# Kernel optimization log

Hardware: AMD Instinct MI355X
Metric: run time of the kernel (lower is better)

The kernel has to match this reference:

```python
import jax, jax.numpy as jnp
import numpy as np

K_HEADS, D_HEAD = 8, 8
D = K_HEADS * D_HEAD  # 64


def _fc(x, W, b=None, relu=False):
    # 1x1 Conv2D over (B,T,N,C) == per-position dense
    y = x @ W
    if b is not None:
        y = y + b
    return jax.nn.relu(y) if relu else y


def _split_heads(x):
    # (B,T,N,K*d) -> (K,B,T,N,d); matches torch.cat(torch.split(x, d, -1), 0)
    B, T, N, _ = x.shape
    return x.reshape(B, T, N, K_HEADS, D_HEAD).transpose(3, 0, 1, 2, 4)


def _merge_heads(x):
    # (K,B,T,N,d) -> (B,T,N,K*d); matches torch.cat(torch.split(x, B, 0), -1)
    K, B, T, N, d = x.shape
    return x.transpose(1, 2, 3, 0, 4).reshape(B, T, N, K * d)


def _forward(X, TLE, key_padding_mask, *P):
    (sa_Wq, sa_bq, sa_Wk, sa_bk, sa_Wv, sa_bv, sa_Wo1, sa_bo1, sa_Wo2, sa_bo2,
     ta_Wq, ta_bq, ta_Wk, ta_bk, ta_Wv, ta_bv, ta_Wo1, ta_bo1, ta_Wo2, ta_bo2,
     g_Wxs, g_Wxt, g_bxt, g_Wh1, g_bh1, g_Wh2, g_bh2) = P
    B, T, N, _ = X.shape
    scale = 1.0 / (D_HEAD ** 0.5)
    XE = jnp.concatenate([X, TLE], axis=-1)  # (B,T,N,3D)

    # ---- Spatial attention (over nodes) ----
    q = _split_heads(_fc(XE, sa_Wq, sa_bq, True))
    k = _split_heads(_fc(XE, sa_Wk, sa_bk, True))
    v = _split_heads(_fc(XE, sa_Wv, sa_bv, True))
    s = jnp.einsum('kbtnd,kbtmd->kbtnm', q, k) * scale  # (K,B,T,N,N)
    p = jax.nn.softmax(s, axis=-1)
    HS = _merge_heads(jnp.einsum('kbtnm,kbtmd->kbtnd', p, v))
    HS = _fc(_fc(HS, sa_Wo1, sa_bo1, True), sa_Wo2, sa_bo2)

    # ---- Temporal attention (over time, causal + key padding) ----
    q = _split_heads(_fc(XE, ta_Wq, ta_bq, True))
    k = _split_heads(_fc(XE, ta_Wk, ta_bk, True))
    v = _split_heads(_fc(XE, ta_Wv, ta_bv, True))
    s = jnp.einsum('kbind,kbjnd->kbnij', q, k) * scale  # (K,B,N,T,T)
    causal = jnp.tril(jnp.ones((T, T), dtype=bool))  # (T,T)
    valid_key = jnp.arange(T)[None, :] < key_padding_mask  # (B,T)
    m = causal[None, None, None] & valid_key[None, :, None, None, :]
    s = jnp.where(m, s, -jnp.inf)
    p = jax.nn.softmax(s, axis=-1)
    HT = _merge_heads(jnp.einsum('kbnij,kbjnd->kbind', p, v))
    HT = _fc(_fc(HT, ta_Wo1, ta_bo1, True), ta_Wo2, ta_bo2)

    # ---- Gated fusion + residual ----
    z = jax.nn.sigmoid(HS @ g_Wxs + HT @ g_Wxt + g_bxt)
    H = z * HS + (1.0 - z) * HT
    H = _fc(_fc(H, g_Wh1, g_bh1, True), g_Wh2, g_bh2)
    return X + H


_PARAM_SHAPES = []
for _pre in ('sa', 'ta'):
    _PARAM_SHAPES += [(_pre + '_Wq', (3 * D, D)), (_pre + '_bq', (D,)),
                      (_pre + '_Wk', (3 * D, D)), (_pre + '_bk', (D,)),
                      (_pre + '_Wv', (3 * D, D)), (_pre + '_bv', (D,)),
                      (_pre + '_Wo1', (D, D)), (_pre + '_bo1', (D,)),
                      (_pre + '_Wo2', (D, D)), (_pre + '_bo2', (D,))]
_PARAM_SHAPES += [('g_Wxs', (D, D)), ('g_Wxt', (D, D)), ('g_bxt', (D,)),
                  ('g_Wh1', (D, D)), ('g_bh1', (D,)),
                  ('g_Wh2', (D, D)), ('g_bh2', (D,))]


def setup_inputs() -> dict:
    key = jax.random.key(0)
    ks = jax.random.split(key, 3 + len(_PARAM_SHAPES))
    B, T, N = 16, 24, 128
    inp = {
        'X': jax.random.normal(ks[0], (B, T, N, D), dtype=jnp.float32),
        'TLE': jax.random.normal(ks[1], (B, T, N, 2 * D), dtype=jnp.float32),
        'key_padding_mask': jax.random.randint(ks[2], (B, 1), 1, T + 1),
    }
    for i, (nm, shp) in enumerate(_PARAM_SHAPES):
        inp[nm] = jax.random.normal(ks[3 + i], shp, dtype=jnp.float32) * 0.05
    return inp


def reference(X, TLE, key_padding_mask,
              sa_Wq, sa_bq, sa_Wk, sa_bk, sa_Wv, sa_bv, sa_Wo1, sa_bo1, sa_Wo2, sa_bo2,
              ta_Wq, ta_bq, ta_Wk, ta_bk, ta_Wv, ta_bv, ta_Wo1, ta_bo1, ta_Wo2, ta_bo2,
              g_Wxs, g_Wxt, g_bxt, g_Wh1, g_bh1, g_Wh2, g_bh2):
    return _forward(X, TLE, key_padding_mask,
                    sa_Wq, sa_bq, sa_Wk, sa_bk, sa_Wv, sa_bv, sa_Wo1, sa_bo1, sa_Wo2, sa_bo2,
                    ta_Wq, ta_bq, ta_Wk, ta_bk, ta_Wv, ta_bv, ta_Wo1, ta_bo1, ta_Wo2, ta_bo2,
                    g_Wxs, g_Wxt, g_bxt, g_Wh1, g_bh1, g_Wh2, g_bh2)
```

## Files before the change

kernel.cpp:

```cpp
#include <hip/hip_runtime.h>
#include <math.h>

#define BB 16
#define TT 24
#define NN 128
#define DD 64
#define PTOT (BB * TT * NN)
#define P64  (PTOT * 64)

typedef __attribute__((ext_vector_type(8))) short bf16x8;
typedef __attribute__((ext_vector_type(4))) float f32x4;
typedef __attribute__((ext_vector_type(16))) float f32x16;

__device__ __forceinline__ unsigned short f2bf(float f) {
    unsigned u = __builtin_bit_cast(unsigned, f);
    u = (u + 0x7fffu + ((u >> 16) & 1u)) >> 16;
    return (unsigned short)u;
}
__device__ __forceinline__ unsigned cvt_pk_bf16(float a, float b) {
    unsigned r;
    asm("v_cvt_pk_bf16_f32 %0, %1, %2" : "=v"(r) : "v"(a), "v"(b));
    return r;
}
__device__ __forceinline__ void unpack8(uint4 u, float* f) {
    f[0] = __builtin_bit_cast(float, u.x << 16);
    f[1] = __builtin_bit_cast(float, u.x & 0xFFFF0000u);
    f[2] = __builtin_bit_cast(float, u.y << 16);
    f[3] = __builtin_bit_cast(float, u.y & 0xFFFF0000u);
    f[4] = __builtin_bit_cast(float, u.z << 16);
    f[5] = __builtin_bit_cast(float, u.z & 0xFFFF0000u);
    f[6] = __builtin_bit_cast(float, u.w << 16);
    f[7] = __builtin_bit_cast(float, u.w & 0xFFFF0000u);
}
__device__ __forceinline__ uint4 pack8(const float* f) {
    uint4 o;
    o.x = cvt_pk_bf16(f[0], f[1]);
    o.y = cvt_pk_bf16(f[2], f[3]);
    o.z = cvt_pk_bf16(f[4], f[5]);
    o.w = cvt_pk_bf16(f[6], f[7]);
    return o;
}
__device__ __forceinline__ float fast_exp2(float x) {
#if __has_builtin(__builtin_amdgcn_exp2f)
    return __builtin_amdgcn_exp2f(x);
#else
    return exp2f(x);
#endif
}
__device__ __forceinline__ f32x16 zero16() {
    f32x16 z;
    #pragma unroll
    for (int i = 0; i < 16; ++i) z[i] = 0.f;
    return z;
}

__global__ __launch_bounds__(256) void wprep_all(
    const float* __restrict__ W0, const float* __restrict__ W1,
    const float* __restrict__ W2, const float* __restrict__ W3,
    const float* __restrict__ W4, const float* __restrict__ W5,
    const float* __restrict__ E0, const float* __restrict__ E1,
    const float* __restrict__ E2, const float* __restrict__ E3,
    const float* __restrict__ E4, const float* __restrict__ E5,
    const float* __restrict__ E6, const float* __restrict__ E7,
    unsigned short* __restrict__ Wt, unsigned short* __restrict__ Wt8)
{
    const int bid = blockIdx.x;
    if (bid < 288) {
        const float* Ws[6] = {W0, W1, W2, W3, W4, W5};
        const int e = bid * 256 + threadIdx.x;
        const int j = e / 12288;
        const int r = e % 12288;
        const int k = r / 64;
        const int n = r % 64;
        Wt[j * 12288 + n * 192 + k] = f2bf(Ws[j][k * 64 + n]);
    } else {
        const float* Es[8] = {E0, E1, E2, E3, E4, E5, E6, E7};
        const int e = (bid - 288) * 256 + threadIdx.x;
        const int mat = e >> 12;
        const int r = e & 4095;
        const int k = r >> 6;
        const int n = r & 63;
        Wt8[mat * 4096 + n * 64 + k] = f2bf(Es[mat][k * 64 + n]);
    }
}

__global__ __launch_bounds__(512, 2) void fused_sattn(
    const float* __restrict__ X, const float* __restrict__ TLE,
    const unsigned short* __restrict__ Wt,
    const float* __restrict__ b0, const float* __restrict__ b1,
    const float* __restrict__ b2, const float* __restrict__ b3,
    const float* __restrict__ b4, const float* __restrict__ b5,
    unsigned short* __restrict__ qt, unsigned short* __restrict__ kt,
    unsigned short* __restrict__ vt,
    unsigned short* __restrict__ HS)
{
    __shared__ __align__(16) unsigned short xe[2][16][200];
    __shared__ __align__(16) unsigned short qq[128 * 64];
    __shared__ __align__(16) unsigned short kk[128 * 64];
    __shared__ __align__(16) unsigned short vvT[64 * 128];
    const int tid = threadIdx.x;
    const long p0 = (long)blockIdx.x * 128;
    const int w = tid >> 6, l = tid & 63, quad = l >> 4, l16 = l & 15;
    const int nt = w >> 1;
    const int mg = (w & 1) * 3;

    int mj[3], kj[3];
    const float* srcb[3];
    long rstride[3];
    #pragma unroll
    for (int j = 0; j < 3; ++j) {
        const int f = (j * 512 + tid) * 2;
        mj[j] = f / 192;
        kj[j] = f % 192;
        if (kj[j] < 64) { srcb[j] = X + (p0 + mj[j]) * 64 + kj[j];  rstride[j] = 16 * 64; }
        else            { srcb[j] = TLE + (p0 + mj[j]) * 128 + (kj[j] - 64); rstride[j] = 16 * 128; }
    }

    uint2 t0a, t0b, t0c, t1a, t1b, t1c, t2a, t2b, t2c, t3a, t3b, t3c,
          t4a, t4b, t4c, t5a, t5b, t5c, t6a, t6b, t6c, t7a, t7b, t7c;
#define LOADT(T, A, B, C) \
    A = *reinterpret_cast<const uint2*>(srcb[0] + (long)(T) * rstride[0]); \
    B = *reinterpret_cast<const uint2*>(srcb[1] + (long)(T) * rstride[1]); \
    C = *reinterpret_cast<const uint2*>(srcb[2] + (long)(T) * rstride[2]);
    LOADT(0, t0a, t0b, t0c)
    LOADT(1, t1a, t1b, t1c)
    LOADT(2, t2a, t2b, t2c)
    LOADT(3, t3a, t3b, t3c)
    LOADT(4, t4a, t4b, t4c)
    LOADT(5, t5a, t5b, t5c)
    LOADT(6, t6a, t6b, t6c)
    LOADT(7, t7a, t7b, t7c)
#undef LOADT

    auto swr = [&](uint2 a, uint2 b, uint2 c, int buf) {
        *reinterpret_cast<unsigned*>(&xe[buf][mj[0]][kj[0]]) =
            cvt_pk_bf16(__builtin_bit_cast(float, a.x), __builtin_bit_cast(float, a.y));
        *reinterpret_cast<unsigned*>(&xe[buf][mj[1]][kj[1]]) =
            cvt_pk_bf16(__builtin_bit_cast(float, b.x), __builtin_bit_cast(float, b.y));
        *reinterpret_cast<unsigned*>(&xe[buf][mj[2]][kj[2]]) =
            cvt_pk_bf16(__builtin_bit_cast(float, c.x), __builtin_bit_cast(float, c.y));
    };

    bf16x8 wf[3][6];
    #pragma unroll
    for (int mi = 0; mi < 3; ++mi)
        #pragma unroll
        for (int kc = 0; kc < 6; ++kc)
            wf[mi][kc] = *reinterpret_cast<const bf16x8*>(
                &Wt[(mg + mi) * 12288 + (nt * 16 + l16) * 192 + kc * 32 + quad * 8]);

    const float* bias_p[6] = {b0, b1, b2, b3, b4, b5};
    float4 bias[3];
    #pragma unroll
    for (int mi = 0; mi < 3; ++mi)
        bias[mi] = *reinterpret_cast<const float4*>(&bias_p[mg + mi][nt * 16 + quad * 4]);

    swr(t0a, t0b, t0c, 0);
    __syncthreads();

    const int chBase = nt * 16 + quad * 4;
    const int chunkW = nt * 2 + (quad >> 1);
    const int chSub  = (quad & 1) * 4;
    const float cs = 0.35355339059327373f * 1.4426950408889634f;

    #pragma unroll
    for (int mt = 0; mt < 8; ++mt) {
        switch (mt) {
            case 0: swr(t1a, t1b, t1c, 1); break;
            case 1: swr(t2a, t2b, t2c, 0); break;
            case 2: swr(t3a, t3b, t3c, 1); break;
            case 3: swr(t4a, t4b, t4c, 0); break;
            case 4: swr(t5a, t5b, t5c, 1); break;
            case 5: swr(t6a, t6b, t6c, 0); break;
            case 6: swr(t7a, t7b, t7c, 1); break;
            default: break;
        }

        bf16x8 A[6];
        #pragma unroll
        for (int kc = 0; kc < 6; ++kc)
            A[kc] = *reinterpret_cast<const bf16x8*>(
                &xe[mt & 1][l16][kc * 32 + quad * 8]);

        f32x4 acc[3];
        #pragma unroll
        for (int mi = 0; mi < 3; ++mi)
            acc[mi] = (f32x4){bias[mi].x, bias[mi].y, bias[mi].z, bias[mi].w};
        #pragma unroll
        for (int kc = 0; kc < 6; ++kc)
            #pragma unroll
            for (int mi = 0; mi < 3; ++mi)
                acc[mi] = __builtin_amdgcn_mfma_f32_16x16x32_bf16(
                    wf[mi][kc], A[kc], acc[mi], 0, 0, 0);

        const int pos = mt * 16 + l16;
        if (mg == 0) {
            const int sw = pos * 64 + ((chunkW ^ (pos & 7)) << 3) + chSub;
            uint2 uq;
            uq.x = cvt_pk_bf16(fmaxf(acc[0][0], 0.f) * cs, fmaxf(acc[0][1], 0.f) * cs);
            uq.y = cvt_pk_bf16(fmaxf(acc[0][2], 0.f) * cs, fmaxf(acc[0][3], 0.f) * cs);
            *reinterpret_cast<uint2*>(&qq[sw]) = uq;
            uint2 uk;
            uk.x = cvt_pk_bf16(fmaxf(acc[1][0], 0.f), fmaxf(acc[1][1], 0.f));
            uk.y = cvt_pk_bf16(fmaxf(acc[1][2], 0.f), fmaxf(acc[1][3], 0.f));
            *reinterpret_cast<uint2*>(&kk[sw]) = uk;
            const unsigned pv0 = cvt_pk_bf16(fmaxf(acc[2][0], 0.f), fmaxf(acc[2][1], 0.f));
            const unsigned pv1 = cvt_pk_bf16(fmaxf(acc[2][2], 0.f), fmaxf(acc[2][3], 0.f));
            vvT[(chBase + 0) * 128 + (pos ^ (((chBase + 0) & 7) << 3))] = (unsigned short)pv0;
            vvT[(chBase + 1) * 128 + (pos ^ (((chBase + 1) & 7) << 3))] = (unsigned short)(pv0 >> 16);
            vvT[(chBase + 2) * 128 + (pos ^ (((chBase + 2) & 7) << 3))] = (unsigned short)pv1;
            vvT[(chBase + 3) * 128 + (pos ^ (((chBase + 3) & 7) << 3))] = (unsigned short)(pv1 >> 16);
        } else {
            unsigned short* dstT[3] = {qt, kt, vt};
            const long gp = (p0 + pos) * 64 + chBase;
            #pragma unroll
            for (int mi = 0; mi < 3; ++mi) {
                uint2 u;
                u.x = cvt_pk_bf16(fmaxf(acc[mi][0], 0.f), fmaxf(acc[mi][1], 0.f));
                u.y = cvt_pk_bf16(fmaxf(acc[mi][2], 0.f), fmaxf(acc[mi][3], 0.f));
                *reinterpret_cast<uint2*>(&dstT[mi][gp]) = u;
            }
        }
        __builtin_amdgcn_sched_barrier(0);
        asm volatile("s_waitcnt lgkmcnt(0)" ::: "memory");
        __builtin_amdgcn_s_barrier();
        __builtin_amdgcn_sched_barrier(0);
    }

    const int h  = w;
    const int hi = l >> 5;
    const int ln = l & 31;
    bf16x8 zf = {};
    const int swz = (h ^ (ln & 7)) << 3;

    auto pvstep = [&](f32x16& st, const bf16x8& va0, const bf16x8& va1,
                      f32x16& oacc) {
        const unsigned P0 = cvt_pk_bf16(st[0],  st[1]);
        const unsigned P1 = cvt_pk_bf16(st[2],  st[3]);
        const unsigned P2 = cvt_pk_bf16(st[4],  st[5]);
        const unsigned P3 = cvt_pk_bf16(st[6],  st[7]);
        const unsigned P4 = cvt_pk_bf16(st[8],  st[9]);
        const unsigned P5 = cvt_pk_bf16(st[10], st[11]);
        const unsigned P6 = cvt_pk_bf16(st[12], st[13]);
        const unsigned P7 = cvt_pk_bf16(st[14], st[15]);
        const unsigned V0 = __shfl_xor(hi ? P0 : P2, 32);
        const unsigned V1 = __shfl_xor(hi ? P1 : P3, 32);
        const unsigned V2 = __shfl_xor(hi ? P4 : P6, 32);
        const unsigned V3 = __shfl_xor(hi ? P5 : P7, 32);
        uint4 fe, fo;
        fe.x = hi ? V0 : P0; fe.y = hi ? V1 : P1;
        fe.z = hi ? P2 : V0; fe.w = hi ? P3 : V1;
        fo.x = hi ? V2 : P4; fo.y = hi ? V3 : P5;
        fo.z = hi ? P6 : V2; fo.w = hi ? P7 : V3;
        oacc = __builtin_amdgcn_mfma_f32_32x32x16_bf16(
            va0, __builtin_bit_cast(bf16x8, fe), oacc, 0, 0, 0);
        oacc = __builtin_amdgcn_mfma_f32_32x32x16_bf16(
            va1, __builtin_bit_cast(bf16x8, fo), oacc, 0, 0, 0);
    };

    bf16x8 kf[4];
    #pragma unroll
    for (int t = 0; t < 4; ++t)
        kf[t] = hi ? zf : *reinterpret_cast<const bf16x8*>(&kk[(t * 32 + ln) * 64 + swz]);

    bf16x8 vf[8];
    #pragma unroll
    for (int c = 0; c < 8; ++c) {
        bf16x8 f = zf;
        if (ln < 8) {
            const int base = (h * 8 + ln) * 128 + ((c * 16 + hi * 8) ^ (ln << 3));
            f = *reinterpret_cast<const bf16x8*>(&vvT[base]);
        }
        vf[c] = f;
    }

    #pragma unroll
    for (int ntq = 0; ntq < 4; ++ntq) {
        const int qrow = ntq * 32 + ln;
        bf16x8 qf = hi ? zf : *reinterpret_cast<const bf16x8*>(&qq[qrow * 64 + swz]);

        float sum = 0.f;
        f32x16 oacc = zero16();
        #pragma unroll
        for (int t = 0; t < 4; ++t) {
            f32x16 st = zero16();
            st = __builtin_amdgcn_mfma_f32_32x32x16_bf16(kf[t], qf, st, 0, 0, 0);
            #pragma unroll
            for (int r = 0; r < 16; ++r) { st[r] = fast_exp2(st[r]); sum += st[r]; }
            pvstep(st, vf[2 * t], vf[2 * t + 1], oacc);
        }
        sum += __shfl_xor(sum, 32);

        const float inv = 1.0f / sum;
        uint2 u;
        u.x = cvt_pk_bf16(oacc[0] * inv, oacc[1] * inv);
        u.y = cvt_pk_bf16(oacc[2] * inv, oacc[3] * inv);
        *reinterpret_cast<uint2*>(&HS[(p0 + qrow) * 64 + h * 8 + hi * 4]) = u;
    }
}

__global__ __launch_bounds__(192) void tattn_kernel(
    const unsigned short* __restrict__ Q, const unsigned short* __restrict__ Kb,
    const unsigned short* __restrict__ V, const int* __restrict__ kpm,
    unsigned short* __restrict__ O)
{
    __shared__ float kk[8][TT][8];
    __shared__ float vv[8][TT][8];
    const int tid = threadIdx.x;
    const int n = blockIdx.x & (NN - 1);
    const int b = blockIdx.x >> 7;

    {
        const int hs = tid / TT;
        const int j  = tid % TT;
        const long g = (((long)(b * TT + j)) * NN + n) * 64 + hs * 8;
        uint4 ku = *reinterpret_cast<const uint4*>(&Kb[g]);
        uint4 vu = *reinterpret_cast<const uint4*>(&V[g]);
        float kf[8], vf[8];
        unpack8(ku, kf); unpack8(vu, vf);
        #pragma unroll
        for (int d = 0; d < 8; ++d) { kk[hs][j][d] = kf[d]; vv[hs][j][d] = vf[d]; }
    }

    const int h = tid / TT;
    const int i = tid % TT;
    const long qb = (((long)(b * TT + i)) * NN + n) * 64 + h * 8;
    float q[8];
    {
        uint4 qu = *reinterpret_cast<const uint4*>(&Q[qb]);
        unpack8(qu, q);
    }
    __syncthreads();

    const int kp = kpm[b];
    const float scale = 0.35355339059327373f;

    float s[TT];
    #pragma unroll
    for (int j = 0; j < TT; ++j) {
        float t = 0.0f;
        #pragma unroll
        for (int d = 0; d < 8; ++d) t = fmaf(q[d], kk[h][j][d], t);
        s[j] = (j <= i && j < kp) ? t * scale : -INFINITY;
    }
    float mx = -INFINITY;
    #pragma unroll
    for (int j = 0; j < TT; ++j) mx = fmaxf(mx, s[j]);

    float sum = 0.0f;
    float acc[8];
    #pragma unroll
    for (int d = 0; d < 8; ++d) acc[d] = 0.0f;
    #pragma unroll
    for (int j = 0; j < TT; ++j) {
        const float e = __expf(s[j] - mx);
        sum += e;
        #pragma unroll
        for (int d = 0; d < 8; ++d) acc[d] = fmaf(e, vv[h][j][d], acc[d]);
    }
    const float inv = 1.0f / sum;
    float o[8];
    #pragma unroll
    for (int d = 0; d < 8; ++d) o[d] = acc[d] * inv;
    *reinterpret_cast<uint4*>(&O[qb]) = pack8(o);
}

__global__ __launch_bounds__(256) void epi_kernel(
    const float* __restrict__ X,
    const unsigned short* __restrict__ HSb, const unsigned short* __restrict__ HTb,
    const unsigned short* __restrict__ Wt8,
    const float* __restrict__ sbo1, const float* __restrict__ sbo2,
    const float* __restrict__ tbo1, const float* __restrict__ tbo2,
    const float* __restrict__ bxt,
    const float* __restrict__ bh1, const float* __restrict__ bh2,
    float* __restrict__ out)
{
    constexpr int RS = 72;
    __shared__ __align__(16) unsigned short bufA[64][RS], bufB[64][RS];
    __shared__ __align__(16) unsigned short bufC[64][RS], bufD[64][RS];
    const int tid = threadIdx.x;
    const long p0 = (long)blockIdx.x * 64;
    const int w = tid >> 6, l = tid & 63, quad = l >> 4, l16 = l & 15;
    const int chBase = w * 16 + quad * 4;

    #pragma unroll
    for (int i = 0; i < 4; ++i) {
        const int idx = tid + i * 256;
        const int m = idx >> 4;
        const int c = (idx & 15) * 4;
        *reinterpret_cast<ushort4*>(&bufA[m][c]) =
            *reinterpret_cast<const ushort4*>(&HSb[(p0 + m) * 64 + c]);
        *reinterpret_cast<ushort4*>(&bufC[m][c]) =
            *reinterpret_cast<const ushort4*>(&HTb[(p0 + m) * 64 + c]);
    }
    __syncthreads();

    auto gemm = [&](const unsigned short (*in)[RS], int mat,
                    const float* __restrict__ bias, f32x4* accO) {
        bf16x8 af[2];
        #pragma unroll
        for (int kc = 0; kc < 2; ++kc)
            af[kc] = *reinterpret_cast<const bf16x8*>(
                &Wt8[mat * 4096 + (w * 16 + l16) * 64 + kc * 32 + quad * 8]);
        const float4 b4 = *reinterpret_cast<const float4*>(&bias[chBase]);
        #pragma unroll
        for (int pt = 0; pt < 4; ++pt) {
            f32x4 acc = (f32x4){b4.x, b4.y, b4.z, b4.w};
            #pragma unroll
            for (int kc = 0; kc < 2; ++kc) {
                bf16x8 bf = *reinterpret_cast<const bf16x8*>(
                    &in[pt * 16 + l16][kc * 32 + quad * 8]);
                acc = __builtin_amdgcn_mfma_f32_16x16x32_bf16(af[kc], bf, acc, 0, 0, 0);
            }
            accO[pt] = acc;
        }
    };

    auto writeBuf = [&](unsigned short (*dst)[RS], const f32x4* v, bool relu) {
        #pragma unroll
        for (int pt = 0; pt < 4; ++pt) {
            float a0 = v[pt][0], a1 = v[pt][1], a2 = v[pt][2], a3 = v[pt][3];
            if (relu) { a0 = fmaxf(a0, 0.f); a1 = fmaxf(a1, 0.f);
                        a2 = fmaxf(a2, 0.f); a3 = fmaxf(a3, 0.f); }
            uint2 u;
            u.x = cvt_pk_bf16(a0, a1);
            u.y = cvt_pk_bf16(a2, a3);
            *reinterpret_cast<uint2*>(&dst[pt * 16 + l16][chBase]) = u;
        }
    };

    f32x4 tS[4], tT[4], HSr[4], HTr[4];

    gemm(bufA, 0, sbo1, tS);
    gemm(bufC, 2, tbo1, tT);
    __syncthreads();
    writeBuf(bufB, tS, true);
    writeBuf(bufD, tT, true);
    __syncthreads();

    gemm(bufB, 1, sbo2, HSr);
    gemm(bufD, 3, tbo2, HTr);
    __syncthreads();
    writeBuf(bufA, HSr, false);
    writeBuf(bufC, HTr, false);
    __syncthreads();

    {
        bf16x8 afS[2], afT[2];
        #pragma unroll
        for (int kc = 0; kc < 2; ++kc) {
            afS[kc] = *reinterpret_cast<const bf16x8*>(
                &Wt8[4 * 4096 + (w * 16 + l16) * 64 + kc * 32 + quad * 8]);
            afT[kc] = *reinterpret_cast<const bf16x8*>(
                &Wt8[5 * 4096 + (w * 16 + l16) * 64 + kc * 32 + quad * 8]);
        }
        const float4 b4 = *reinterpret_cast<const float4*>(&bxt[chBase]);
        #pragma unroll
        for (int pt = 0; pt < 4; ++pt) {
            f32x4 acc = (f32x4){b4.x, b4.y, b4.z, b4.w};
            #pragma unroll
            for (int kc = 0; kc < 2; ++kc) {
                bf16x8 hsf = *reinterpret_cast<const bf16x8*>(
                    &bufA[pt * 16 + l16][kc * 32 + quad * 8]);
                acc = __builtin_amdgcn_mfma_f32_16x16x32_bf16(afS[kc], hsf, acc, 0, 0, 0);
            }
            #pragma unroll
            for (int kc = 0; kc < 2; ++kc) {
                bf16x8 htf = *reinterpret_cast<const bf16x8*>(
                    &bufC[pt * 16 + l16][kc * 32 + quad * 8]);
                acc = __builtin_amdgcn_mfma_f32_16x16x32_bf16(afT[kc], htf, acc, 0, 0, 0);
            }
            f32x4 h;
            #pragma unroll
            for (int r = 0; r < 4; ++r) {
                const float z = 1.0f / (1.0f + __expf(-acc[r]));
                h[r] = z * HSr[pt][r] + (1.0f - z) * HTr[pt][r];
            }
            tS[pt] = h;
        }
    }
    writeBuf(bufB, tS, false);
    __syncthreads();

    gemm(bufB, 6, bh1, tS);
    __syncthreads();
    writeBuf(bufA, tS, true);
    __syncthreads();

    gemm(bufA, 7, bh2, tS);
    #pragma unroll
    for (int pt = 0; pt < 4; ++pt) {
        const long pos = p0 + pt * 16 + l16;
        const float4 xv = *reinterpret_cast<const float4*>(&X[pos * 64 + chBase]);
        float4 o;
        o.x = tS[pt][0] + xv.x; o.y = tS[pt][1] + xv.y;
        o.z = tS[pt][2] + xv.z; o.w = tS[pt][3] + xv.w;
        *reinterpret_cast<float4*>(&out[pos * 64 + chBase]) = o;
    }
}

extern "C" void kernel_launch(void* const* d_in, const int* in_sizes, int n_in,
                              void* d_out, int out_size, void* d_ws, size_t ws_size,
                              hipStream_t stream) {
    const float* X   = (const float*)d_in[0];
    const float* TLE = (const float*)d_in[1];
    const int* kpm   = (const int*)d_in[2];

    const float* sa_Wq = (const float*)d_in[3];  const float* sa_bq = (const float*)d_in[4];
    const float* sa_Wk = (const float*)d_in[5];  const float* sa_bk = (const float*)d_in[6];
    const float* sa_Wv = (const float*)d_in[7];  const float* sa_bv = (const float*)d_in[8];
    const float* sa_Wo1 = (const float*)d_in[9];  const float* sa_bo1 = (const float*)d_in[10];
    const float* sa_Wo2 = (const float*)d_in[11]; const float* sa_bo2 = (const float*)d_in[12];
    const float* ta_Wq = (const float*)d_in[13]; const float* ta_bq = (const float*)d_in[14];
    const float* ta_Wk = (const float*)d_in[15]; const float* ta_bk = (const float*)d_in[16];
    const float* ta_Wv = (const float*)d_in[17]; const float* ta_bv = (const float*)d_in[18];
    const float* ta_Wo1 = (const float*)d_in[19]; const float* ta_bo1 = (const float*)d_in[20];
    const float* ta_Wo2 = (const float*)d_in[21]; const float* ta_bo2 = (const float*)d_in[22];
    const float* g_Wxs = (const float*)d_in[23];
    const float* g_Wxt = (const float*)d_in[24]; const float* g_bxt = (const float*)d_in[25];
    const float* g_Wh1 = (const float*)d_in[26]; const float* g_bh1 = (const float*)d_in[27];
    const float* g_Wh2 = (const float*)d_in[28]; const float* g_bh2 = (const float*)d_in[29];

    unsigned short* wsp = (unsigned short*)d_ws;
    unsigned short* qt  = wsp + 0L * P64;
    unsigned short* kt  = wsp + 1L * P64;
    unsigned short* vt  = wsp + 2L * P64;
    unsigned short* HSb = wsp + 3L * P64;
    unsigned short* HTb = wsp + 4L * P64;
    unsigned short* Wt  = wsp + 5L * P64;
    unsigned short* Wt8 = Wt + 6 * 12288;

    float* out = (float*)d_out;

    hipLaunchKernelGGL(wprep_all, dim3(416), dim3(256), 0, stream,
                       sa_Wq, sa_Wk, sa_Wv, ta_Wq, ta_Wk, ta_Wv,
                       sa_Wo1, sa_Wo2, ta_Wo1, ta_Wo2, g_Wxs, g_Wxt, g_Wh1, g_Wh2,
                       Wt, Wt8);

    hipLaunchKernelGGL(fused_sattn, dim3(BB * TT), dim3(512), 0, stream,
                       X, TLE, Wt,
                       sa_bq, sa_bk, sa_bv, ta_bq, ta_bk, ta_bv,
                       qt, kt, vt, HSb);

    hipLaunchKernelGGL(tattn_kernel, dim3(BB * NN), dim3(192), 0, stream,
                       qt, kt, vt, kpm, HTb);

    hipLaunchKernelGGL(epi_kernel, dim3(PTOT / 64), dim3(256), 0, stream,
                       X, HSb, HTb, Wt8,
                       sa_bo1, sa_bo2, ta_bo1, ta_bo2, g_bxt, g_bh1, g_bh2,
                       out);
}
```

Before: 69.15 us.

## Pack four nodes per temporal-attention block and raise wave priority in sattn

The temporal attention kernel now handles four neighbouring nodes per block with 768 threads instead of one node per 192-thread block. This cuts the block count by four and lets each block's loads of adjacent node rows share contiguous memory. Separately, the spatial attention phase of fused_sattn raises wave priority with s_setprio so its MFMA/softmax section is favoured over co-resident waves. The larger blocks use more shared memory each and may reduce scheduling flexibility.

```diff
diff --git a/kernel.cpp b/kernel.cpp
--- a/kernel.cpp
+++ b/kernel.cpp
@@ -227,6 +227,7 @@
         __builtin_amdgcn_sched_barrier(0);
     }
 
+    __builtin_amdgcn_s_setprio(1);
     const int h  = w;
     const int hi = l >> 5;
     const int ln = l & 31;
@@ -297,34 +298,37 @@
         u.y = cvt_pk_bf16(oacc[2] * inv, oacc[3] * inv);
         *reinterpret_cast<uint2*>(&HS[(p0 + qrow) * 64 + h * 8 + hi * 4]) = u;
     }
-}
-
-__global__ __launch_bounds__(192) void tattn_kernel(
+    __builtin_amdgcn_s_setprio(0);
+}
+
+__global__ __launch_bounds__(768) void tattn_kernel(
     const unsigned short* __restrict__ Q, const unsigned short* __restrict__ Kb,
     const unsigned short* __restrict__ V, const int* __restrict__ kpm,
     unsigned short* __restrict__ O)
 {
-    __shared__ float kk[8][TT][8];
-    __shared__ float vv[8][TT][8];
+    __shared__ float kk[4][8][TT][8];
+    __shared__ float vv[4][8][TT][8];
     const int tid = threadIdx.x;
-    const int n = blockIdx.x & (NN - 1);
-    const int b = blockIdx.x >> 7;
+    const int np = tid / 192;
+    const int r  = tid % 192;
+    const int n0 = (blockIdx.x & 31) * 4;
+    const int b  = blockIdx.x >> 5;
 
     {
-        const int hs = tid / TT;
-        const int j  = tid % TT;
-        const long g = (((long)(b * TT + j)) * NN + n) * 64 + hs * 8;
+        const int hs = r / TT;
+        const int j  = r % TT;
+        const long g = (((long)(b * TT + j)) * NN + n0 + np) * 64 + hs * 8;
         uint4 ku = *reinterpret_cast<const uint4*>(&Kb[g]);
         uint4 vu = *reinterpret_cast<const uint4*>(&V[g]);
         float kf[8], vf[8];
         unpack8(ku, kf); unpack8(vu, vf);
         #pragma unroll
-        for (int d = 0; d < 8; ++d) { kk[hs][j][d] = kf[d]; vv[hs][j][d] = vf[d]; }
-    }
-
-    const int h = tid / TT;
-    const int i = tid % TT;
-    const long qb = (((long)(b * TT + i)) * NN + n) * 64 + h * 8;
+        for (int d = 0; d < 8; ++d) { kk[np][hs][j][d] = kf[d]; vv[np][hs][j][d] = vf[d]; }
+    }
+
+    const int h = r / TT;
+    const int i = r % TT;
+    const long qb = (((long)(b * TT + i)) * NN + n0 + np) * 64 + h * 8;
     float q[8];
     {
         uint4 qu = *reinterpret_cast<const uint4*>(&Q[qb]);
@@ -340,7 +344,7 @@
     for (int j = 0; j < TT; ++j) {
         float t = 0.0f;
         #pragma unroll
-        for (int d = 0; d < 8; ++d) t = fmaf(q[d], kk[h][j][d], t);
+        for (int d = 0; d < 8; ++d) t = fmaf(q[d], kk[np][h][j][d], t);
         s[j] = (j <= i && j < kp) ? t * scale : -INFINITY;
     }
     float mx = -INFINITY;
@@ -356,7 +360,7 @@
         const float e = __expf(s[j] - mx);
         sum += e;
         #pragma unroll
-        for (int d = 0; d < 8; ++d) acc[d] = fmaf(e, vv[h][j][d], acc[d]);
+        for (int d = 0; d < 8; ++d) acc[d] = fmaf(e, vv[np][h][j][d], acc[d]);
     }
     const float inv = 1.0f / sum;
     float o[8];
@@ -542,7 +546,7 @@
                        sa_bq, sa_bk, sa_bv, ta_bq, ta_bk, ta_bv,
                        qt, kt, vt, HSb);
 
-    hipLaunchKernelGGL(tattn_kernel, dim3(BB * NN), dim3(192), 0, stream,
+    hipLaunchKernelGGL(tattn_kernel, dim3(BB * NN / 4), dim3(768), 0, stream,
                        qt, kt, vt, kpm, HTb);
 
     hipLaunchKernelGGL(epi_kernel, dim3(PTOT / 64), dim3(256), 0, stream,
```

Result: no change. 69.66 us (+0.7%).
